# Optimization experiments

Measured on AMD Instinct MI355X. Metric: run time of the kernel, lower is better.

Reference implementation:

```python
import jax, jax.numpy as jnp
import numpy as np

HIDDEN_D = 1024
MAP_D = 2048


def lstm_cell(x, h, c, W_ih, W_hh, b_ih, b_hh):
    # PyTorch LSTMCell: gates ordered (i, f, g, o)
    gates = x @ W_ih.T + b_ih + h @ W_hh.T + b_hh  # [1, 4H]
    i, f, g, o = jnp.split(gates, 4, axis=-1)
    i = jax.nn.sigmoid(i)
    f = jax.nn.sigmoid(f)
    g = jnp.tanh(g)
    o = jax.nn.sigmoid(o)
    c_new = f * c + i * g
    h_new = o * jnp.tanh(c_new)
    return h_new, c_new


def setup_inputs() -> dict:
    key = jax.random.key(0)
    ks = jax.random.split(key, 16)
    H = HIDDEN_D
    s = 1.0 / np.sqrt(H)  # PyTorch LSTMCell init scale
    inp = {
        "goal_point": jax.random.normal(ks[0], (2,), jnp.float32),
        "current_point": jax.random.normal(ks[1], (2,), jnp.float32),
        "map": jax.random.normal(ks[2], (1, MAP_D), jnp.float32),
        # lstm_map: input_size = MAP_D
        "W_ih_map": jax.random.uniform(ks[3], (4 * H, MAP_D), jnp.float32, -s, s),
        "W_hh_map": jax.random.uniform(ks[4], (4 * H, H), jnp.float32, -s, s),
        "b_ih_map": jax.random.uniform(ks[5], (4 * H,), jnp.float32, -s, s),
        "b_hh_map": jax.random.uniform(ks[6], (4 * H,), jnp.float32, -s, s),
        # lstm_points: input_size = 4
        "W_ih_pts": jax.random.uniform(ks[7], (4 * H, 4), jnp.float32, -s, s),
        "W_hh_pts": jax.random.uniform(ks[8], (4 * H, H), jnp.float32, -s, s),
        "b_ih_pts": jax.random.uniform(ks[9], (4 * H,), jnp.float32, -s, s),
        "b_hh_pts": jax.random.uniform(ks[10], (4 * H,), jnp.float32, -s, s),
        # lstm1: input_size = 2H
        "W_ih_1": jax.random.uniform(ks[11], (4 * H, 2 * H), jnp.float32, -s, s),
        "W_hh_1": jax.random.uniform(ks[12], (4 * H, H), jnp.float32, -s, s),
        "b_ih_1": jax.random.uniform(ks[13], (4 * H,), jnp.float32, -s, s),
        "b_hh_1": jax.random.uniform(ks[14], (4 * H,), jnp.float32, -s, s),
        # fc: H -> 2
        "fc_w": jax.random.uniform(ks[15], (2, H), jnp.float32, -s, s),
        "fc_b": jnp.zeros((2,), jnp.float32),
    }
    return inp


def reference(goal_point, current_point, map,
              W_ih_map, W_hh_map, b_ih_map, b_hh_map,
              W_ih_pts, W_hh_pts, b_ih_pts, b_hh_pts,
              W_ih_1, W_hh_1, b_ih_1, b_hh_1,
              fc_w, fc_b):
    H = W_hh_map.shape[1]
    z = jnp.zeros((1, H), map.dtype)  # init_hidden: all-zero states
    points = jnp.concatenate([current_point, goal_point], axis=0)[None, :]  # [1, 4]

    h_map, _ = lstm_cell(map, z, z, W_ih_map, W_hh_map, b_ih_map, b_hh_map)
    h_pts, _ = lstm_cell(points, z, z, W_ih_pts, W_hh_pts, b_ih_pts, b_hh_pts)
    final_in = jnp.concatenate([h_map, h_pts], axis=1)  # [1, 2H]
    h1, _ = lstm_cell(final_in, z, z, W_ih_1, W_hh_1, b_ih_1, b_hh_1)
    # dropout disabled (deterministic reference / eval mode)
    output = h1 @ fc_w.T + fc_b  # [1, 2]
    return output
```

## Files before the change

kernel.cpp:

```cpp
#include <hip/hip_runtime.h>
#include <math.h>

#define H    1024
#define D2   2048

typedef float f32x4 __attribute__((ext_vector_type(4)));

__device__ __forceinline__ float sigmoidf_(float x) {
    return 1.0f / (1.0f + expf(-x));
}

__device__ __forceinline__ float wave_sum(float v) {
#pragma unroll
    for (int off = 32; off >= 1; off >>= 1)
        v += __shfl_xor(v, off, 64);
    return v;
}

__device__ __forceinline__ void gemv3_deep(
    const f32x4* __restrict__ x4,
    const f32x4* __restrict__ Wi,
    const f32x4* __restrict__ Wg,
    const f32x4* __restrict__ Wo,
    int lane, float& si, float& sg, float& so)
{
    f32x4 xv[8], wa[8], wg[8], wo[8];
#pragma unroll
    for (int it = 0; it < 8; ++it) xv[it] = x4[it * 64 + lane];
#pragma unroll
    for (int it = 0; it < 8; ++it) wa[it] = Wi[it * 64 + lane];
#pragma unroll
    for (int it = 0; it < 8; ++it) wg[it] = Wg[it * 64 + lane];
#pragma unroll
    for (int it = 0; it < 8; ++it) wo[it] = Wo[it * 64 + lane];

    float a = 0.f, b = 0.f, c = 0.f;
#pragma unroll
    for (int it = 0; it < 8; ++it) {
        a += wa[it].x * xv[it].x + wa[it].y * xv[it].y + wa[it].z * xv[it].z + wa[it].w * xv[it].w;
        b += wg[it].x * xv[it].x + wg[it].y * xv[it].y + wg[it].z * xv[it].z + wg[it].w * xv[it].w;
        c += wo[it].x * xv[it].x + wo[it].y * xv[it].y + wo[it].z * xv[it].z + wo[it].w * xv[it].w;
    }
    si = wave_sum(a);
    sg = wave_sum(b);
    so = wave_sum(c);
}

__global__ __launch_bounds__(256, 1) void k_first(
    const float* __restrict__ x,
    const float* __restrict__ W,
    const float* __restrict__ b_ih,
    const float* __restrict__ b_hh,
    const float* __restrict__ Wp,
    const float* __restrict__ bp_ih,
    const float* __restrict__ bp_hh,
    const float* __restrict__ goal,
    const float* __restrict__ cur,
    float* __restrict__ fin)
{
    int b = blockIdx.x;
    if (b < 256) {
        int wave = threadIdx.x >> 6;
        int lane = threadIdx.x & 63;
        int j = b * 4 + wave;
        float si, sg, so;
        gemv3_deep((const f32x4*)x,
                   (const f32x4*)(W + (size_t)j * D2),
                   (const f32x4*)(W + (size_t)(2 * H + j) * D2),
                   (const f32x4*)(W + (size_t)(3 * H + j) * D2),
                   lane, si, sg, so);
        if (lane == 0) {
            float gi = si + b_ih[j] + b_hh[j];
            float gg = sg + b_ih[2 * H + j] + b_hh[2 * H + j];
            float go = so + b_ih[3 * H + j] + b_hh[3 * H + j];
            float c = sigmoidf_(gi) * tanhf(gg);
            fin[j] = sigmoidf_(go) * tanhf(c);
        }
    } else {
        float p0 = cur[0], p1 = cur[1], p2 = goal[0], p3 = goal[1];
        const f32x4* Wp4 = (const f32x4*)Wp;
#pragma unroll
        for (int t = 0; t < 4; ++t) {
            int j = t * 256 + threadIdx.x;
            f32x4 wi = Wp4[j];
            f32x4 wg = Wp4[2 * H + j];
            f32x4 wo = Wp4[3 * H + j];
            float gi = wi.x * p0 + wi.y * p1 + wi.z * p2 + wi.w * p3 + bp_ih[j] + bp_hh[j];
            float gg = wg.x * p0 + wg.y * p1 + wg.z * p2 + wg.w * p3 + bp_ih[2 * H + j] + bp_hh[2 * H + j];
            float go = wo.x * p0 + wo.y * p1 + wo.z * p2 + wo.w * p3 + bp_ih[3 * H + j] + bp_hh[3 * H + j];
            float c = sigmoidf_(gi) * tanhf(gg);
            fin[H + j] = sigmoidf_(go) * tanhf(c);
        }
    }
}

__global__ __launch_bounds__(256, 1) void k_lstm1(
    const float* __restrict__ fin,
    const float* __restrict__ W1,
    const float* __restrict__ b1_i,
    const float* __restrict__ b1_h,
    float* __restrict__ h1)
{
    int wave = threadIdx.x >> 6;
    int lane = threadIdx.x & 63;
    int j = blockIdx.x * 4 + wave;
    float si, sg, so;
    gemv3_deep((const f32x4*)fin,
               (const f32x4*)(W1 + (size_t)j * D2),
               (const f32x4*)(W1 + (size_t)(2 * H + j) * D2),
               (const f32x4*)(W1 + (size_t)(3 * H + j) * D2),
               lane, si, sg, so);
    if (lane == 0) {
        float gi = si + b1_i[j] + b1_h[j];
        float gg = sg + b1_i[2 * H + j] + b1_h[2 * H + j];
        float go = so + b1_i[3 * H + j] + b1_h[3 * H + j];
        float c = sigmoidf_(gi) * tanhf(gg);
        h1[j] = sigmoidf_(go) * tanhf(c);
    }
}

__global__ __launch_bounds__(128) void k_fc(
    const float* __restrict__ h1,
    const float* __restrict__ fcw,
    const float* __restrict__ fcb,
    float* __restrict__ out)
{
    int wave = threadIdx.x >> 6;
    int lane = threadIdx.x & 63;
    float s = 0.f;
#pragma unroll
    for (int k = 0; k < 16; ++k) {
        int idx = k * 64 + lane;
        s += h1[idx] * fcw[wave * H + idx];
    }
    s = wave_sum(s);
    if (lane == 0) out[wave] = s + fcb[wave];
}

extern "C" void kernel_launch(void* const* d_in, const int* in_sizes, int n_in,
                              void* d_out, int out_size, void* d_ws, size_t ws_size,
                              hipStream_t stream) {
    const float* goal     = (const float*)d_in[0];
    const float* cur      = (const float*)d_in[1];
    const float* map      = (const float*)d_in[2];
    const float* W_ih_map = (const float*)d_in[3];
    const float* b_ih_map = (const float*)d_in[5];
    const float* b_hh_map = (const float*)d_in[6];
    const float* W_ih_pts = (const float*)d_in[7];
    const float* b_ih_pts = (const float*)d_in[9];
    const float* b_hh_pts = (const float*)d_in[10];
    const float* W_ih_1   = (const float*)d_in[11];
    const float* b_ih_1   = (const float*)d_in[13];
    const float* b_hh_1   = (const float*)d_in[14];
    const float* fc_w     = (const float*)d_in[15];
    const float* fc_b     = (const float*)d_in[16];

    float* fin = (float*)d_ws;
    float* h1  = (float*)d_ws + 2048;
    float* out = (float*)d_out;

    k_first<<<257, 256, 0, stream>>>(map, W_ih_map, b_ih_map, b_hh_map,
                                     W_ih_pts, b_ih_pts, b_hh_pts,
                                     goal, cur, fin);
    k_lstm1<<<256, 256, 0, stream>>>(fin, W_ih_1, b_ih_1, b_hh_1, h1);
    k_fc<<<1, 128, 0, stream>>>(h1, fc_w, fc_b, out);
}
```

Baseline: 18.99 us.

## Fuse final FC layer into LSTM1 kernel via last-block atomic reduction

```diff
diff --git a/kernel.cpp b/kernel.cpp
--- a/kernel.cpp
+++ b/kernel.cpp
@@ -3,6 +3,7 @@
 
 #define H    1024
 #define D2   2048
+#define NB2  256
 
 typedef float f32x4 __attribute__((ext_vector_type(4)));
 
@@ -56,6 +57,7 @@
     const float* __restrict__ bp_hh,
     const float* __restrict__ goal,
     const float* __restrict__ cur,
+    unsigned*    __restrict__ cnt,
     float* __restrict__ fin)
 {
     int b = blockIdx.x;
@@ -77,6 +79,9 @@
             fin[j] = sigmoidf_(go) * tanhf(c);
         }
     } else {
+        if (threadIdx.x == 0) {
+            __hip_atomic_store(&cnt[0], 0u, __ATOMIC_RELAXED, __HIP_MEMORY_SCOPE_AGENT);
+        }
         float p0 = cur[0], p1 = cur[1], p2 = goal[0], p3 = goal[1];
         const f32x4* Wp4 = (const f32x4*)Wp;
 #pragma unroll
@@ -94,16 +99,25 @@
     }
 }
 
-__global__ __launch_bounds__(256, 1) void k_lstm1(
+__global__ __launch_bounds__(256, 1) void k_l1fc(
     const float* __restrict__ fin,
     const float* __restrict__ W1,
     const float* __restrict__ b1_i,
     const float* __restrict__ b1_h,
-    float* __restrict__ h1)
+    const float* __restrict__ fcw,
+    const float* __restrict__ fcb,
+    unsigned*    __restrict__ cnt,
+    float*       __restrict__ pbuf,
+    float* __restrict__ out)
 {
-    int wave = threadIdx.x >> 6;
-    int lane = threadIdx.x & 63;
-    int j = blockIdx.x * 4 + wave;
+    const int tid  = threadIdx.x;
+    const int wave = tid >> 6;
+    const int lane = tid & 63;
+    const int j    = blockIdx.x * 4 + wave;
+
+    __shared__ float    hs0[4], hs1[4];
+    __shared__ unsigned slast;
+
     float si, sg, so;
     gemv3_deep((const f32x4*)fin,
                (const f32x4*)(W1 + (size_t)j * D2),
@@ -115,26 +129,38 @@
         float gg = sg + b1_i[2 * H + j] + b1_h[2 * H + j];
         float go = so + b1_i[3 * H + j] + b1_h[3 * H + j];
         float c = sigmoidf_(gi) * tanhf(gg);
-        h1[j] = sigmoidf_(go) * tanhf(c);
+        float h = sigmoidf_(go) * tanhf(c);
+        hs0[wave] = h * fcw[j];
+        hs1[wave] = h * fcw[H + j];
     }
-}
+    __syncthreads();
 
-__global__ __launch_bounds__(128) void k_fc(
-    const float* __restrict__ h1,
-    const float* __restrict__ fcw,
-    const float* __restrict__ fcb,
-    float* __restrict__ out)
-{
-    int wave = threadIdx.x >> 6;
-    int lane = threadIdx.x & 63;
-    float s = 0.f;
+    if (tid == 0) {
+        float p0 = hs0[0] + hs0[1] + hs0[2] + hs0[3];
+        float p1 = hs1[0] + hs1[1] + hs1[2] + hs1[3];
+        __hip_atomic_store(&pbuf[2 * blockIdx.x],     p0, __ATOMIC_RELAXED, __HIP_MEMORY_SCOPE_AGENT);
+        __hip_atomic_store(&pbuf[2 * blockIdx.x + 1], p1, __ATOMIC_RELAXED, __HIP_MEMORY_SCOPE_AGENT);
+        asm volatile("s_waitcnt vmcnt(0)" ::: "memory");
+        unsigned old = __hip_atomic_fetch_add(&cnt[0], 1u, __ATOMIC_RELAXED, __HIP_MEMORY_SCOPE_AGENT);
+        slast = (old == NB2 - 1) ? 1u : 0u;
+    }
+    __syncthreads();
+
+    if (slast && wave == 0) {
+        float s0 = 0.f, s1 = 0.f;
 #pragma unroll
-    for (int k = 0; k < 16; ++k) {
-        int idx = k * 64 + lane;
-        s += h1[idx] * fcw[wave * H + idx];
+        for (int i = 0; i < 4; ++i) {
+            int b = i * 64 + lane;
+            s0 += __hip_atomic_load(&pbuf[2 * b],     __ATOMIC_RELAXED, __HIP_MEMORY_SCOPE_AGENT);
+            s1 += __hip_atomic_load(&pbuf[2 * b + 1], __ATOMIC_RELAXED, __HIP_MEMORY_SCOPE_AGENT);
+        }
+        s0 = wave_sum(s0);
+        s1 = wave_sum(s1);
+        if (lane == 0) {
+            out[0] = s0 + fcb[0];
+            out[1] = s1 + fcb[1];
+        }
     }
-    s = wave_sum(s);
-    if (lane == 0) out[wave] = s + fcb[wave];
 }
 
 extern "C" void kernel_launch(void* const* d_in, const int* in_sizes, int n_in,
@@ -155,13 +181,14 @@
     const float* fc_w     = (const float*)d_in[15];
     const float* fc_b     = (const float*)d_in[16];
 
-    float* fin = (float*)d_ws;
-    float* h1  = (float*)d_ws + 2048;
-    float* out = (float*)d_out;
+    unsigned* cnt  = (unsigned*)d_ws;
+    float*    pbuf = (float*)((char*)d_ws + 64);
+    float*    fin  = (float*)((char*)d_ws + 4096);
+    float*    out  = (float*)d_out;
 
     k_first<<<257, 256, 0, stream>>>(map, W_ih_map, b_ih_map, b_hh_map,
                                      W_ih_pts, b_ih_pts, b_hh_pts,
-                                     goal, cur, fin);
-    k_lstm1<<<256, 256, 0, stream>>>(fin, W_ih_1, b_ih_1, b_hh_1, h1);
-    k_fc<<<1, 128, 0, stream>>>(h1, fc_w, fc_b, out);
+                                     goal, cur, cnt, fin);
+    k_l1fc<<<NB2, 256, 0, stream>>>(fin, W_ih_1, b_ih_1, b_hh_1,
+                                    fc_w, fc_b, cnt, pbuf, out);
 }
```

After: 20.75 us. 9.3% more time.
